# Performance work log

Hardware: AMD Instinct MI355X
Metric: run time of the kernel (lower is better)

Reference implementation:

```python
import jax, jax.numpy as jnp
import numpy as np

B, N, DIM = 2, 2048, 1024
HEADS, DH, NUM_MEM = 8, 64, 4
EPS = 1e-5


def layer_norm(x, gamma):
    mu = x.mean(-1, keepdims=True)
    var = ((x - mu) ** 2).mean(-1, keepdims=True)
    return (x - mu) * jax.lax.rsqrt(var + EPS) * gamma


def setup_inputs() -> dict:
    key = jax.random.key(0)
    ks = jax.random.split(key, 7)
    x = jax.random.normal(ks[0], (B, N, DIM), jnp.float32)
    mask = jax.random.randint(ks[1], (B, N), 0, 2) > 0
    attn_bias = jax.random.normal(ks[2], (HEADS, N, N), jnp.float32) * 0.02
    gamma = jnp.ones((DIM,), jnp.float32)
    Wq = jax.random.normal(ks[3], (DIM, HEADS * DH), jnp.float32) * (DIM ** -0.5)
    Wkv = jax.random.normal(ks[4], (DIM, 2 * DH), jnp.float32) * (DIM ** -0.5)
    mem_kv = jax.random.normal(ks[5], (2, NUM_MEM, DH), jnp.float32)
    Wout = jax.random.normal(ks[6], (HEADS * DH, DIM), jnp.float32) * ((HEADS * DH) ** -0.5)
    return dict(x=x, attn_bias=attn_bias, gamma=gamma, Wq=Wq, Wkv=Wkv,
                mem_kv=mem_kv, Wout=Wout, mask=mask)


def reference(x, attn_bias, gamma, Wq, Wkv, mem_kv, Wout, mask):
    b, n, _ = x.shape
    # norm applied to query path only; kv comes from pre-norm x (self-attention)
    xn = layer_norm(x, gamma)
    q = (xn @ Wq).reshape(b, n, HEADS, DH).transpose(0, 2, 1, 3) * (DH ** -0.5)  # b h n d
    kv = x @ Wkv  # multi-query: single shared kv head
    k, v = kv[..., :DH], kv[..., DH:]
    mk = jnp.broadcast_to(mem_kv[0], (b, NUM_MEM, DH))
    mv = jnp.broadcast_to(mem_kv[1], (b, NUM_MEM, DH))
    k = jnp.concatenate([mk, k], axis=1)  # b (m+n) d
    v = jnp.concatenate([mv, v], axis=1)
    j = n + NUM_MEM
    bias = jnp.pad(attn_bias, ((0, 0), (0, 0), (NUM_MEM, 0)))  # zero bias on mem tokens
    maskp = jnp.pad(mask, ((0, 0), (NUM_MEM, 0)), constant_values=True)
    sim = jnp.einsum('bhid,bjd->bhij', q, k) + bias
    neg = -jnp.finfo(sim.dtype).max
    sim = jnp.where(maskp[:, None, None, :], sim, neg)
    causal = jnp.triu(jnp.ones((n, j), bool), k=NUM_MEM + 1)  # mem tokens always visible
    sim = jnp.where(causal, neg, sim)
    attn = jax.nn.softmax(sim, axis=-1)
    out = jnp.einsum('bhij,bjd->bhid', attn, v)
    out = out.transpose(0, 2, 1, 3).reshape(b, n, HEADS * DH)
    return out @ Wout
```

## Files before the change

kernel.cpp:

```cpp
#include <hip/hip_runtime.h>
#include <hip/hip_bf16.h>
#include <float.h>

#define B_ 2
#define N_ 2048
#define DIM_ 1024
#define HEADS_ 8
#define DH_ 64
#define NUM_MEM_ 4
#define ROWS_ (B_ * N_)
#define QCOLS_ (HEADS_ * DH_)
#define JTOT_ (N_ + NUM_MEM_)
#define JPAD_ 2176
#define CHUNKS_PER_BH_ 77

typedef __attribute__((ext_vector_type(8))) short short8v;
typedef __attribute__((ext_vector_type(4))) float f32x4;

static __device__ __forceinline__ ushort f2b(float f) {
    __hip_bfloat16 hb = __float2bfloat16(f);
    return *(ushort*)&hb;
}
static __device__ __forceinline__ uint pk2(float a, float b) {
    return ((uint)f2b(b) << 16) | (uint)f2b(a);
}
static __device__ __forceinline__ float b2f_lo(uint u) {
    union { uint x; float f; } c; c.x = u << 16; return c.f;
}
static __device__ __forceinline__ float b2f_hi(uint u) {
    union { uint x; float f; } c; c.x = u & 0xffff0000u; return c.f;
}

__global__ __launch_bounds__(256) void ln_cast_kernel(const float* __restrict__ x,
                                                      const float* __restrict__ gamma,
                                                      ushort* __restrict__ xb,
                                                      ushort* __restrict__ xnb) {
    int row = blockIdx.x;
    const float4 v = ((const float4*)(x + (size_t)row * DIM_))[threadIdx.x];
    float s  = v.x + v.y + v.z + v.w;
    float s2 = v.x * v.x + v.y * v.y + v.z * v.z + v.w * v.w;
    #pragma unroll
    for (int off = 32; off > 0; off >>= 1) {
        s  += __shfl_down(s, off);
        s2 += __shfl_down(s2, off);
    }
    __shared__ float ws1[4], ws2[4];
    int lane = threadIdx.x & 63, wid = threadIdx.x >> 6;
    if (lane == 0) { ws1[wid] = s; ws2[wid] = s2; }
    __syncthreads();
    float tot  = ws1[0] + ws1[1] + ws1[2] + ws1[3];
    float tot2 = ws2[0] + ws2[1] + ws2[2] + ws2[3];
    float mu  = tot * (1.0f / DIM_);
    float var = tot2 * (1.0f / DIM_) - mu * mu;
    float rs  = rsqrtf(var + 1e-5f);
    const float4 g = ((const float4*)gamma)[threadIdx.x];
    float vv[4] = {v.x, v.y, v.z, v.w};
    float gg[4] = {g.x, g.y, g.z, g.w};
    ushort xo[4], xno[4];
    #pragma unroll
    for (int j = 0; j < 4; ++j) {
        xo[j]  = f2b(vv[j]);
        xno[j] = f2b((vv[j] - mu) * rs * gg[j]);
    }
    *(int2*)(xb  + (size_t)row * DIM_ + threadIdx.x * 4) = *(int2*)xo;
    *(int2*)(xnb + (size_t)row * DIM_ + threadIdx.x * 4) = *(int2*)xno;
}

static __device__ __forceinline__ void wtrans_body(const float* __restrict__ W,
                                                   ushort* __restrict__ Wt,
                                                   int K, int N, int t) {
    int n = t % N;
    int k0 = (t / N) * 8;
    ushort u[8];
    #pragma unroll
    for (int j = 0; j < 8; ++j) u[j] = f2b(W[(size_t)(k0 + j) * N + n]);
    *(int4*)(Wt + (size_t)n * K + k0) = *(int4*)u;
}

__global__ __launch_bounds__(256) void prep_kernel(const float* __restrict__ Wq,
                                                   const float* __restrict__ Wkv,
                                                   const float* __restrict__ Wout,
                                                   const float* __restrict__ mem_kv,
                                                   const int* __restrict__ mask,
                                                   ushort* __restrict__ Wqt,
                                                   ushort* __restrict__ Wkvt,
                                                   ushort* __restrict__ Woutt,
                                                   ushort* __restrict__ Kb,
                                                   ushort* __restrict__ Vt,
                                                   ushort* __restrict__ amask) {
    int bid = blockIdx.x;
    int tid = threadIdx.x;
    if (bid < 256) {
        wtrans_body(Wq, Wqt, DIM_, QCOLS_, bid * 256 + tid);
    } else if (bid < 320) {
        wtrans_body(Wkv, Wkvt, DIM_, 2 * DH_, (bid - 256) * 256 + tid);
    } else if (bid < 576) {
        wtrans_body(Wout, Woutt, QCOLS_, DIM_, (bid - 320) * 256 + tid);
    } else if (bid < 640) {
        int t = (bid - 576) * 256 + tid;
        int d  = t & 63;
        int ji = (t >> 6) & 127;
        int b  = t >> 13;
        int j  = (ji < NUM_MEM_) ? ji : (2048 + ji);
        float kv_ = 0.f, vv = 0.f;
        if (ji < NUM_MEM_) {
            kv_ = mem_kv[ji * DH_ + d];
            vv  = mem_kv[NUM_MEM_ * DH_ + ji * DH_ + d];
        }
        Kb[((size_t)(b * JPAD_) + j) * DH_ + d] = f2b(kv_);
        Vt[((size_t)(b * DH_) + d) * JPAD_ + j] = f2b(vv);
    } else {
        int t = (bid - 640) * 256 + tid;
        if (t < B_ * JPAD_) {
            int b = t / JPAD_;
            int j = t % JPAD_;
            float v;
            if (j < NUM_MEM_) v = 0.f;
            else if (j < JTOT_) v = mask[b * N_ + (j - NUM_MEM_)] ? 0.f : -1e30f;
            else v = -1e30f;
            amask[(size_t)b * JPAD_ + j] = f2b(v);
        }
    }
}

template<int MODE, int BM>
__global__ __launch_bounds__(256) void gemm_bf16(const ushort* __restrict__ A,
                                                 const ushort* __restrict__ Bt,
                                                 void* __restrict__ C,
                                                 void* __restrict__ C2,
                                                 int M, int N, int K) {
    constexpr int RT = BM / 64;
    __shared__ ushort As[BM][40];
    __shared__ ushort Bs[64][40];
    int tid = threadIdx.x;
    int w = tid >> 6, l = tid & 63, lg = l >> 4, ll = l & 15;
    int r0 = blockIdx.y * BM, c0 = blockIdx.x * 64;

    int arow = tid >> 2;
    int achk = (tid & 3) * 8;
    const ushort* Ap  = A + (size_t)(r0 + arow) * K + achk;
    const ushort* Ap2 = Ap + (size_t)64 * K;
    const ushort* Bp  = Bt + (size_t)(c0 + arow) * K + achk;

    int4 a0 = *(const int4*)Ap;
    int4 a1;
    if constexpr (RT == 2) a1 = *(const int4*)Ap2;
    int4 b0 = *(const int4*)Bp;

    f32x4 acc[RT][4] = {};

    int nk = K / 32;
    for (int ks = 0; ks < nk; ++ks) {
        __syncthreads();
        *(int4*)&As[arow][achk] = a0;
        if constexpr (RT == 2) *(int4*)&As[arow + 64][achk] = a1;
        *(int4*)&Bs[arow][achk] = b0;
        __syncthreads();
        int kn = (ks + 1 < nk) ? (ks + 1) * 32 : 0;
        a0 = *(const int4*)(Ap + kn);
        if constexpr (RT == 2) a1 = *(const int4*)(Ap2 + kn);
        b0 = *(const int4*)(Bp + kn);
        short8v af[RT], bf[4];
        #pragma unroll
        for (int rt = 0; rt < RT; ++rt)
            af[rt] = *(const short8v*)&As[w * 16 * RT + rt * 16 + ll][lg * 8];
        #pragma unroll
        for (int ct = 0; ct < 4; ++ct)
            bf[ct] = *(const short8v*)&Bs[ct * 16 + ll][lg * 8];
        __builtin_amdgcn_s_setprio(1);
        #pragma unroll
        for (int rt = 0; rt < RT; ++rt)
            #pragma unroll
            for (int ct = 0; ct < 4; ++ct)
                acc[rt][ct] = __builtin_amdgcn_mfma_f32_16x16x32_bf16(af[rt], bf[ct], acc[rt][ct], 0, 0, 0);
        __builtin_amdgcn_s_setprio(0);
    }

    #pragma unroll
    for (int rt = 0; rt < RT; ++rt) {
        #pragma unroll
        for (int ct = 0; ct < 4; ++ct) {
            #pragma unroll
            for (int r = 0; r < 4; ++r) {
                int row = r0 + w * 16 * RT + rt * 16 + lg * 4 + r;
                int col = c0 + ct * 16 + ll;
                float val = acc[rt][ct][r];
                if (MODE == 0) {
                    ((ushort*)C)[(size_t)row * QCOLS_ + col] = f2b(val * 0.125f);
                } else if (MODE == 1) {
                    int b = row >> 11;
                    int j = (row & 2047) + NUM_MEM_;
                    if (col < DH_)
                        ((ushort*)C)[((size_t)(b * JPAD_) + j) * DH_ + col] = f2b(val);
                    else
                        ((ushort*)C2)[((size_t)(b * DH_) + (col - DH_)) * JPAD_ + j] = f2b(val);
                } else {
                    ((float*)C)[(size_t)row * DIM_ + col] = val;
                }
            }
        }
    }
}

__global__ __launch_bounds__(256, 4) void fattn_split_kernel(const ushort* __restrict__ qb,
                                                             const ushort* __restrict__ Kb,
                                                             const ushort* __restrict__ Vt,
                                                             const float* __restrict__ bias,
                                                             const ushort* __restrict__ amask,
                                                             ushort* __restrict__ part_O,
                                                             float* __restrict__ part_ml) {
    __shared__ ushort Ks[64][72];
    __shared__ ushort Vs[64][72];
    __shared__ ushort Pt[4][16][72];
    __shared__ ushort Bb[64][68];

    int cid = blockIdx.x;
    int bh  = cid / CHUNKS_PER_BH_;
    int rem = cid - bh * CHUNKS_PER_BH_;
    int b = bh >> 3, h = bh & 7;
    int qt = 0, ci = 0;
    {
        int cum = 0;
        #pragma unroll 1
        for (int t = 0; t < 32; ++t) {
            int c = (t + 10) / 9;
            if (rem < cum + c) { qt = t; ci = rem - cum; break; }
            cum += c;
        }
    }
    int nt = qt + 2;
    int nc = (qt + 10) / 9;
    int t0 = ci * nt / nc;
    int t1 = (ci + 1) * nt / nc;
    int q0 = qt * 64;

    int tid = threadIdx.x;
    int w  = tid >> 6;
    int l  = tid & 63;
    int lg = l >> 4;
    int ll = l & 15;
    int i_row = q0 + w * 16 + ll;

    short8v aq0, aq1;
    {
        const ushort* qp = qb + ((size_t)(b * N_ + i_row)) * QCOLS_ + h * DH_;
        aq0 = *(const short8v*)(qp + lg * 8);
        aq1 = *(const short8v*)(qp + 32 + lg * 8);
    }

    int trow = tid >> 5;
    int tpc  = tid & 31;
    const float*  bias_rb = bias + ((size_t)h * N_ + q0 + trow) * N_;
    const ushort* am_row  = amask + (size_t)b * JPAD_;

    int sr = tid >> 3, sc = (tid & 7) * 8;
    const ushort* KbB = Kb + (size_t)b * JPAD_ * DH_;
    const ushort* VtB = Vt + (size_t)b * DH_ * JPAD_;

    auto fold_bias = [&](const float2* bv, uint am2, uint* bbx) {
        float amf0 = b2f_lo(am2), amf1 = b2f_hi(am2);
        int j_e = 0;
        (void)j_e;
    };
    (void)fold_bias;

    int jp0 = t0 * 64;
    int4 kr0 = *(const int4*)(KbB + (size_t)(jp0 + sr) * DH_ + sc);
    int4 kr1 = *(const int4*)(KbB + (size_t)(jp0 + sr + 32) * DH_ + sc);
    int4 vr0 = *(const int4*)(VtB + (size_t)sr * JPAD_ + jp0 + sc);
    int4 vr1 = *(const int4*)(VtB + (size_t)(sr + 32) * JPAD_ + jp0 + sc);

    uint bbc[8];
    {
        int j_e = jp0 + 2 * tpc;
        int sj  = j_e - NUM_MEM_;
        int sjc = sj < 0 ? 0 : (sj > N_ - 2 ? N_ - 2 : sj);
        uint am2 = *(const uint*)(am_row + j_e);
        float amf0 = b2f_lo(am2), amf1 = b2f_hi(am2);
        #pragma unroll
        for (int p = 0; p < 8; ++p) {
            float2 bv = *(const float2*)(bias_rb + (size_t)(8 * p) * N_ + sjc);
            int i_s = q0 + trow + 8 * p;
            float v0 = (j_e     < NUM_MEM_) ? 0.f : bv.x + amf0;
            float v1 = (j_e + 1 < NUM_MEM_) ? 0.f : bv.y + amf1;
            v0 = (j_e     <= i_s + NUM_MEM_) ? v0 : -1e30f;
            v1 = (j_e + 1 <= i_s + NUM_MEM_) ? v1 : -1e30f;
            bbc[p] = pk2(v0, v1);
        }
    }

    f32x4 oacc[4] = {};
    float mrow1 = -1e30f, lsum1 = 0.f;

    for (int jt = t0; jt < t1; ++jt) {
        __syncthreads();
        *(int4*)&Ks[sr][sc]      = kr0;
        *(int4*)&Ks[sr + 32][sc] = kr1;
        *(int4*)&Vs[sr][sc]      = vr0;
        *(int4*)&Vs[sr + 32][sc] = vr1;
        #pragma unroll
        for (int p = 0; p < 8; ++p)
            *(uint*)&Bb[trow + 8 * p][2 * tpc] = bbc[p];
        __syncthreads();

        int jn0 = (jt + 1 < t1 ? jt + 1 : jt) * 64;
        kr0 = *(const int4*)(KbB + (size_t)(jn0 + sr) * DH_ + sc);
        kr1 = *(const int4*)(KbB + (size_t)(jn0 + sr + 32) * DH_ + sc);
        vr0 = *(const int4*)(VtB + (size_t)sr * JPAD_ + jn0 + sc);
        vr1 = *(const int4*)(VtB + (size_t)(sr + 32) * JPAD_ + jn0 + sc);
        int j_e = jn0 + 2 * tpc;
        int sj  = j_e - NUM_MEM_;
        int sjc = sj < 0 ? 0 : (sj > N_ - 2 ? N_ - 2 : sj);
        uint am2n = *(const uint*)(am_row + j_e);
        float2 bvn[8];
        #pragma unroll
        for (int p = 0; p < 8; ++p)
            bvn[p] = *(const float2*)(bias_rb + (size_t)(8 * p) * N_ + sjc);

        float s[4][4];
        #pragma unroll
        for (int ct = 0; ct < 4; ++ct) {
            f32x4 acc = {};
            short8v bk0 = *(const short8v*)&Ks[ct * 16 + ll][lg * 8];
            short8v bk1 = *(const short8v*)&Ks[ct * 16 + ll][32 + lg * 8];
            __builtin_amdgcn_s_setprio(1);
            acc = __builtin_amdgcn_mfma_f32_16x16x32_bf16(bk0, aq0, acc, 0, 0, 0);
            acc = __builtin_amdgcn_mfma_f32_16x16x32_bf16(bk1, aq1, acc, 0, 0, 0);
            __builtin_amdgcn_s_setprio(0);
            uint2 ub = *(const uint2*)&Bb[w * 16 + ll][ct * 16 + lg * 4];
            s[ct][0] = acc[0] + b2f_lo(ub.x);
            s[ct][1] = acc[1] + b2f_hi(ub.x);
            s[ct][2] = acc[2] + b2f_lo(ub.y);
            s[ct][3] = acc[3] + b2f_hi(ub.y);
        }

        float m01 = fmaxf(fmaxf(s[0][0], s[0][1]), fmaxf(s[0][2], s[0][3]));
        float m23 = fmaxf(fmaxf(s[1][0], s[1][1]), fmaxf(s[1][2], s[1][3]));
        float m45 = fmaxf(fmaxf(s[2][0], s[2][1]), fmaxf(s[2][2], s[2][3]));
        float m67 = fmaxf(fmaxf(s[3][0], s[3][1]), fmaxf(s[3][2], s[3][3]));
        float m = fmaxf(fmaxf(m01, m23), fmaxf(m45, m67));
        m = fmaxf(m, __shfl_xor(m, 16));
        m = fmaxf(m, __shfl_xor(m, 32));
        float mn = fmaxf(mrow1, m);
        float scl = __expf(mrow1 - mn);
        mrow1 = mn;

        float ps = 0.f;
        #pragma unroll
        for (int ct = 0; ct < 4; ++ct)
            #pragma unroll
            for (int r = 0; r < 4; ++r) {
                float p = __expf(s[ct][r] - mn);
                s[ct][r] = p;
                ps += p;
            }
        ps += __shfl_xor(ps, 16);
        ps += __shfl_xor(ps, 32);
        lsum1 = lsum1 * scl + ps;

        #pragma unroll
        for (int ct = 0; ct < 4; ++ct) {
            uint2 pu;
            pu.x = pk2(s[ct][0], s[ct][1]);
            pu.y = pk2(s[ct][2], s[ct][3]);
            *(uint2*)&Pt[w][ll][ct * 16 + lg * 4] = pu;
        }
        #pragma unroll
        for (int dt = 0; dt < 4; ++dt)
            #pragma unroll
            for (int r = 0; r < 4; ++r) oacc[dt][r] *= scl;

        #pragma unroll
        for (int c = 0; c < 2; ++c) {
            short8v ptf = *(const short8v*)&Pt[w][ll][c * 32 + lg * 8];
            __builtin_amdgcn_s_setprio(1);
            #pragma unroll
            for (int dt = 0; dt < 4; ++dt) {
                short8v bv = *(const short8v*)&Vs[dt * 16 + ll][c * 32 + lg * 8];
                oacc[dt] = __builtin_amdgcn_mfma_f32_16x16x32_bf16(bv, ptf, oacc[dt], 0, 0, 0);
            }
            __builtin_amdgcn_s_setprio(0);
        }

        {
            float amf0 = b2f_lo(am2n), amf1 = b2f_hi(am2n);
            #pragma unroll
            for (int p = 0; p < 8; ++p) {
                int i_s = q0 + trow + 8 * p;
                float v0 = (j_e     < NUM_MEM_) ? 0.f : bvn[p].x + amf0;
                float v1 = (j_e + 1 < NUM_MEM_) ? 0.f : bvn[p].y + amf1;
                v0 = (j_e     <= i_s + NUM_MEM_) ? v0 : -1e30f;
                v1 = (j_e + 1 <= i_s + NUM_MEM_) ? v1 : -1e30f;
                bbc[p] = pk2(v0, v1);
            }
        }
    }

    int slot = (bh * 32 + qt) * 4 + ci;
    ushort* po = part_O + (size_t)slot * 4096;
    #pragma unroll
    for (int dt = 0; dt < 4; ++dt) {
        uint2 pu;
        pu.x = pk2(oacc[dt][0], oacc[dt][1]);
        pu.y = pk2(oacc[dt][2], oacc[dt][3]);
        *(uint2*)&po[(w * 16 + ll) * 64 + dt * 16 + lg * 4] = pu;
    }
    if (lg == 0) {
        part_ml[(size_t)slot * 128 + (w * 16 + ll) * 2]     = mrow1;
        part_ml[(size_t)slot * 128 + (w * 16 + ll) * 2 + 1] = lsum1;
    }
}

__global__ __launch_bounds__(256) void merge_kernel(const ushort* __restrict__ part_O,
                                                    const float* __restrict__ part_ml,
                                                    ushort* __restrict__ attn_ob) {
    int bid = blockIdx.x;
    int qt = bid & 31;
    int bh = bid >> 5;
    int b = bh >> 3, h = bh & 7;
    int nc = (qt + 10) / 9;
    int tid = threadIdx.x;
    int row = tid >> 2;
    int dseg = (tid & 3) * 16;
    int slot0 = bid * 4;

    float M = -1e30f;
    #pragma unroll
    for (int c = 0; c < 4; ++c) {
        if (c >= nc) break;
        M = fmaxf(M, part_ml[(size_t)(slot0 + c) * 128 + row * 2]);
    }
    float den = 0.f;
    float num[16] = {};
    #pragma unroll
    for (int c = 0; c < 4; ++c) {
        if (c >= nc) break;
        float m_c = part_ml[(size_t)(slot0 + c) * 128 + row * 2];
        float l_c = part_ml[(size_t)(slot0 + c) * 128 + row * 2 + 1];
        float wgt = __expf(m_c - M);
        den += wgt * l_c;
        const uint4* src = (const uint4*)(part_O + (size_t)(slot0 + c) * 4096 + row * 64 + dseg);
        uint4 v0 = src[0];
        uint uu[8] = { v0.x, v0.y, v0.z, v0.w, 0, 0, 0, 0 };
        uint4 v1 = src[1];
        uu[4] = v1.x; uu[5] = v1.y; uu[6] = v1.z; uu[7] = v1.w;
        #pragma unroll
        for (int e = 0; e < 8; ++e) {
            num[e * 2 + 0] += wgt * b2f_lo(uu[e]);
            num[e * 2 + 1] += wgt * b2f_hi(uu[e]);
        }
    }
    float inv = 1.f / den;
    ushort o[16];
    #pragma unroll
    for (int e = 0; e < 16; ++e) o[e] = f2b(num[e] * inv);
    int i = qt * 64 + row;
    ushort* dst = attn_ob + ((size_t)(b * N_ + i)) * QCOLS_ + h * DH_ + dseg;
    *(int4*)dst = *(int4*)o;
    *(int4*)(dst + 8) = *(int4*)(o + 8);
}

extern "C" void kernel_launch(void* const* d_in, const int* in_sizes, int n_in,
                              void* d_out, int out_size, void* d_ws, size_t ws_size,
                              hipStream_t stream) {
    const float* x         = (const float*)d_in[0];
    const float* attn_bias = (const float*)d_in[1];
    const float* gamma     = (const float*)d_in[2];
    const float* Wq        = (const float*)d_in[3];
    const float* Wkv       = (const float*)d_in[4];
    const float* mem_kv    = (const float*)d_in[5];
    const float* Wout      = (const float*)d_in[6];
    const int*   mask      = (const int*)d_in[7];
    float* out = (float*)d_out;

    char* wsb = (char*)d_ws;
    ushort* xb      = (ushort*)wsb;
    ushort* xnb     = (ushort*)(wsb + (8u  << 20));
    ushort* qb      = (ushort*)(wsb + (16u << 20));
    ushort* attn_ob = (ushort*)(wsb + (20u << 20));
    ushort* Kb      = (ushort*)(wsb + (24u << 20));
    ushort* Vt      = (ushort*)(wsb + (25u << 20));
    ushort* Wqt     = (ushort*)(wsb + (26u << 20));
    ushort* Wkvt    = (ushort*)(wsb + (27u << 20));
    ushort* Woutt   = (ushort*)(wsb + (28u << 20));
    ushort* amask   = (ushort*)(wsb + (29u << 20));
    ushort* part_O  = (ushort*)(wsb + (32u << 20));
    float*  part_ml = (float*)(wsb + (64u << 20));

    ln_cast_kernel<<<ROWS_, 256, 0, stream>>>(x, gamma, xb, xnb);
    prep_kernel<<<657, 256, 0, stream>>>(Wq, Wkv, Wout, mem_kv, mask, Wqt, Wkvt, Woutt, Kb, Vt, amask);

    gemm_bf16<0, 64><<<dim3(QCOLS_ / 64, ROWS_ / 64), 256, 0, stream>>>(xnb, Wqt, qb, nullptr, ROWS_, QCOLS_, DIM_);
    gemm_bf16<1, 64><<<dim3((2 * DH_) / 64, ROWS_ / 64), 256, 0, stream>>>(xb, Wkvt, Kb, Vt, ROWS_, 2 * DH_, DIM_);
    fattn_split_kernel<<<16 * CHUNKS_PER_BH_, 256, 0, stream>>>(qb, Kb, Vt, attn_bias, amask, part_O, part_ml);
    merge_kernel<<<512, 256, 0, stream>>>(part_O, part_ml, attn_ob);
    gemm_bf16<2, 128><<<dim3(DIM_ / 64, ROWS_ / 128), 256, 0, stream>>>(attn_ob, Woutt, out, nullptr, ROWS_, DIM_, QCOLS_);
}
```

Before: 103.2 us.

## Merge launch stages and replace LDS P transpose with lane shuffles

```diff
diff --git a/kernel.cpp b/kernel.cpp
--- a/kernel.cpp
+++ b/kernel.cpp
@@ -31,41 +31,6 @@
     union { uint x; float f; } c; c.x = u & 0xffff0000u; return c.f;
 }
 
-__global__ __launch_bounds__(256) void ln_cast_kernel(const float* __restrict__ x,
-                                                      const float* __restrict__ gamma,
-                                                      ushort* __restrict__ xb,
-                                                      ushort* __restrict__ xnb) {
-    int row = blockIdx.x;
-    const float4 v = ((const float4*)(x + (size_t)row * DIM_))[threadIdx.x];
-    float s  = v.x + v.y + v.z + v.w;
-    float s2 = v.x * v.x + v.y * v.y + v.z * v.z + v.w * v.w;
-    #pragma unroll
-    for (int off = 32; off > 0; off >>= 1) {
-        s  += __shfl_down(s, off);
-        s2 += __shfl_down(s2, off);
-    }
-    __shared__ float ws1[4], ws2[4];
-    int lane = threadIdx.x & 63, wid = threadIdx.x >> 6;
-    if (lane == 0) { ws1[wid] = s; ws2[wid] = s2; }
-    __syncthreads();
-    float tot  = ws1[0] + ws1[1] + ws1[2] + ws1[3];
-    float tot2 = ws2[0] + ws2[1] + ws2[2] + ws2[3];
-    float mu  = tot * (1.0f / DIM_);
-    float var = tot2 * (1.0f / DIM_) - mu * mu;
-    float rs  = rsqrtf(var + 1e-5f);
-    const float4 g = ((const float4*)gamma)[threadIdx.x];
-    float vv[4] = {v.x, v.y, v.z, v.w};
-    float gg[4] = {g.x, g.y, g.z, g.w};
-    ushort xo[4], xno[4];
-    #pragma unroll
-    for (int j = 0; j < 4; ++j) {
-        xo[j]  = f2b(vv[j]);
-        xno[j] = f2b((vv[j] - mu) * rs * gg[j]);
-    }
-    *(int2*)(xb  + (size_t)row * DIM_ + threadIdx.x * 4) = *(int2*)xo;
-    *(int2*)(xnb + (size_t)row * DIM_ + threadIdx.x * 4) = *(int2*)xno;
-}
-
 static __device__ __forceinline__ void wtrans_body(const float* __restrict__ W,
                                                    ushort* __restrict__ Wt,
                                                    int K, int N, int t) {
@@ -77,18 +42,55 @@
     *(int4*)(Wt + (size_t)n * K + k0) = *(int4*)u;
 }
 
-__global__ __launch_bounds__(256) void prep_kernel(const float* __restrict__ Wq,
-                                                   const float* __restrict__ Wkv,
-                                                   const float* __restrict__ Wout,
-                                                   const float* __restrict__ mem_kv,
-                                                   const int* __restrict__ mask,
-                                                   ushort* __restrict__ Wqt,
-                                                   ushort* __restrict__ Wkvt,
-                                                   ushort* __restrict__ Woutt,
-                                                   ushort* __restrict__ Kb,
-                                                   ushort* __restrict__ Vt,
-                                                   ushort* __restrict__ amask) {
-    int bid = blockIdx.x;
+__global__ __launch_bounds__(256) void ln_prep_kernel(const float* __restrict__ x,
+                                                      const float* __restrict__ gamma,
+                                                      const float* __restrict__ Wq,
+                                                      const float* __restrict__ Wkv,
+                                                      const float* __restrict__ Wout,
+                                                      const float* __restrict__ mem_kv,
+                                                      const int* __restrict__ mask,
+                                                      ushort* __restrict__ xb,
+                                                      ushort* __restrict__ xnb,
+                                                      ushort* __restrict__ Wqt,
+                                                      ushort* __restrict__ Wkvt,
+                                                      ushort* __restrict__ Woutt,
+                                                      ushort* __restrict__ Kb,
+                                                      ushort* __restrict__ Vt,
+                                                      ushort* __restrict__ amask) {
+    int bid0 = blockIdx.x;
+    if (bid0 < ROWS_) {
+        int row = bid0;
+        const float4 v = ((const float4*)(x + (size_t)row * DIM_))[threadIdx.x];
+        float s  = v.x + v.y + v.z + v.w;
+        float s2 = v.x * v.x + v.y * v.y + v.z * v.z + v.w * v.w;
+        #pragma unroll
+        for (int off = 32; off > 0; off >>= 1) {
+            s  += __shfl_down(s, off);
+            s2 += __shfl_down(s2, off);
+        }
+        __shared__ float ws1[4], ws2[4];
+        int lane = threadIdx.x & 63, wid = threadIdx.x >> 6;
+        if (lane == 0) { ws1[wid] = s; ws2[wid] = s2; }
+        __syncthreads();
+        float tot  = ws1[0] + ws1[1] + ws1[2] + ws1[3];
+        float tot2 = ws2[0] + ws2[1] + ws2[2] + ws2[3];
+        float mu  = tot * (1.0f / DIM_);
+        float var = tot2 * (1.0f / DIM_) - mu * mu;
+        float rs  = rsqrtf(var + 1e-5f);
+        const float4 g = ((const float4*)gamma)[threadIdx.x];
+        float vv[4] = {v.x, v.y, v.z, v.w};
+        float gg[4] = {g.x, g.y, g.z, g.w};
+        ushort xo[4], xno[4];
+        #pragma unroll
+        for (int j = 0; j < 4; ++j) {
+            xo[j]  = f2b(vv[j]);
+            xno[j] = f2b((vv[j] - mu) * rs * gg[j]);
+        }
+        *(int2*)(xb  + (size_t)row * DIM_ + threadIdx.x * 4) = *(int2*)xo;
+        *(int2*)(xnb + (size_t)row * DIM_ + threadIdx.x * 4) = *(int2*)xno;
+        return;
+    }
+    int bid = bid0 - ROWS_;
     int tid = threadIdx.x;
     if (bid < 256) {
         wtrans_body(Wq, Wqt, DIM_, QCOLS_, bid * 256 + tid);
@@ -123,18 +125,96 @@
     }
 }
 
-template<int MODE, int BM>
-__global__ __launch_bounds__(256) void gemm_bf16(const ushort* __restrict__ A,
-                                                 const ushort* __restrict__ Bt,
-                                                 void* __restrict__ C,
-                                                 void* __restrict__ C2,
-                                                 int M, int N, int K) {
-    constexpr int RT = BM / 64;
-    __shared__ ushort As[BM][40];
+template<int MODE>
+static __device__ __forceinline__ void gemm64_body(ushort (*As)[40], ushort (*Bs)[40],
+                                                   const ushort* __restrict__ A,
+                                                   const ushort* __restrict__ Bt,
+                                                   void* __restrict__ C,
+                                                   void* __restrict__ C2,
+                                                   int N, int K, int bx, int by) {
+    int tid = threadIdx.x;
+    int w = tid >> 6, l = tid & 63, lg = l >> 4, ll = l & 15;
+    int r0 = by * 64, c0 = bx * 64;
+
+    int arow = tid >> 2;
+    int achk = (tid & 3) * 8;
+    const ushort* Ap = A + (size_t)(r0 + arow) * K + achk;
+    const ushort* Bp = Bt + (size_t)(c0 + arow) * K + achk;
+
+    int4 a0 = *(const int4*)Ap;
+    int4 b0 = *(const int4*)Bp;
+
+    f32x4 acc[4] = {};
+
+    int nk = K / 32;
+    for (int ks = 0; ks < nk; ++ks) {
+        __syncthreads();
+        *(int4*)&As[arow][achk] = a0;
+        *(int4*)&Bs[arow][achk] = b0;
+        __syncthreads();
+        int kn = (ks + 1 < nk) ? (ks + 1) * 32 : 0;
+        a0 = *(const int4*)(Ap + kn);
+        b0 = *(const int4*)(Bp + kn);
+        short8v af, bf[4];
+        af = *(const short8v*)&As[w * 16 + ll][lg * 8];
+        #pragma unroll
+        for (int ct = 0; ct < 4; ++ct)
+            bf[ct] = *(const short8v*)&Bs[ct * 16 + ll][lg * 8];
+        __builtin_amdgcn_s_setprio(1);
+        #pragma unroll
+        for (int ct = 0; ct < 4; ++ct)
+            acc[ct] = __builtin_amdgcn_mfma_f32_16x16x32_bf16(af, bf[ct], acc[ct], 0, 0, 0);
+        __builtin_amdgcn_s_setprio(0);
+    }
+
+    #pragma unroll
+    for (int ct = 0; ct < 4; ++ct) {
+        #pragma unroll
+        for (int r = 0; r < 4; ++r) {
+            int row = r0 + w * 16 + lg * 4 + r;
+            int col = c0 + ct * 16 + ll;
+            float val = acc[ct][r];
+            if (MODE == 0) {
+                ((ushort*)C)[(size_t)row * QCOLS_ + col] = f2b(val * 0.125f);
+            } else {
+                int b = row >> 11;
+                int j = (row & 2047) + NUM_MEM_;
+                if (col < DH_)
+                    ((ushort*)C)[((size_t)(b * JPAD_) + j) * DH_ + col] = f2b(val);
+                else
+                    ((ushort*)C2)[((size_t)(b * DH_) + (col - DH_)) * JPAD_ + j] = f2b(val);
+            }
+        }
+    }
+}
+
+__global__ __launch_bounds__(256) void gemm01_kernel(const ushort* __restrict__ xnb,
+                                                     const ushort* __restrict__ Wqt,
+                                                     ushort* __restrict__ qb,
+                                                     const ushort* __restrict__ xb,
+                                                     const ushort* __restrict__ Wkvt,
+                                                     ushort* __restrict__ Kb,
+                                                     ushort* __restrict__ Vt) {
+    __shared__ ushort As[64][40];
+    __shared__ ushort Bs[64][40];
+    int bid = blockIdx.x;
+    if (bid < 512) {
+        gemm64_body<0>(As, Bs, xnb, Wqt, qb, nullptr, QCOLS_, DIM_, bid & 7, bid >> 3);
+    } else {
+        int r = bid - 512;
+        gemm64_body<1>(As, Bs, xb, Wkvt, Kb, Vt, 2 * DH_, DIM_, r & 1, r >> 1);
+    }
+}
+
+__global__ __launch_bounds__(256) void gemm_out_kernel(const ushort* __restrict__ A,
+                                                       const ushort* __restrict__ Bt,
+                                                       float* __restrict__ C,
+                                                       int M, int N, int K) {
+    __shared__ ushort As[128][40];
     __shared__ ushort Bs[64][40];
     int tid = threadIdx.x;
     int w = tid >> 6, l = tid & 63, lg = l >> 4, ll = l & 15;
-    int r0 = blockIdx.y * BM, c0 = blockIdx.x * 64;
+    int r0 = blockIdx.y * 128, c0 = blockIdx.x * 64;
 
     int arow = tid >> 2;
     int achk = (tid & 3) * 8;
@@ -143,33 +223,31 @@
     const ushort* Bp  = Bt + (size_t)(c0 + arow) * K + achk;
 
     int4 a0 = *(const int4*)Ap;
-    int4 a1;
-    if constexpr (RT == 2) a1 = *(const int4*)Ap2;
+    int4 a1 = *(const int4*)Ap2;
     int4 b0 = *(const int4*)Bp;
 
-    f32x4 acc[RT][4] = {};
+    f32x4 acc[2][4] = {};
 
     int nk = K / 32;
     for (int ks = 0; ks < nk; ++ks) {
         __syncthreads();
-        *(int4*)&As[arow][achk] = a0;
-        if constexpr (RT == 2) *(int4*)&As[arow + 64][achk] = a1;
-        *(int4*)&Bs[arow][achk] = b0;
+        *(int4*)&As[arow][achk]      = a0;
+        *(int4*)&As[arow + 64][achk] = a1;
+        *(int4*)&Bs[arow][achk]      = b0;
         __syncthreads();
         int kn = (ks + 1 < nk) ? (ks + 1) * 32 : 0;
         a0 = *(const int4*)(Ap + kn);
-        if constexpr (RT == 2) a1 = *(const int4*)(Ap2 + kn);
+        a1 = *(const int4*)(Ap2 + kn);
         b0 = *(const int4*)(Bp + kn);
-        short8v af[RT], bf[4];
-        #pragma unroll
-        for (int rt = 0; rt < RT; ++rt)
-            af[rt] = *(const short8v*)&As[w * 16 * RT + rt * 16 + ll][lg * 8];
+        short8v af[2], bf[4];
+        af[0] = *(const short8v*)&As[w * 32 + ll][lg * 8];
+        af[1] = *(const short8v*)&As[w * 32 + 16 + ll][lg * 8];
         #pragma unroll
         for (int ct = 0; ct < 4; ++ct)
             bf[ct] = *(const short8v*)&Bs[ct * 16 + ll][lg * 8];
         __builtin_amdgcn_s_setprio(1);
         #pragma unroll
-        for (int rt = 0; rt < RT; ++rt)
+        for (int rt = 0; rt < 2; ++rt)
             #pragma unroll
             for (int ct = 0; ct < 4; ++ct)
                 acc[rt][ct] = __builtin_amdgcn_mfma_f32_16x16x32_bf16(af[rt], bf[ct], acc[rt][ct], 0, 0, 0);
@@ -177,29 +255,15 @@
     }
 
     #pragma unroll
-    for (int rt = 0; rt < RT; ++rt) {
-        #pragma unroll
-        for (int ct = 0; ct < 4; ++ct) {
+    for (int rt = 0; rt < 2; ++rt)
+        #pragma unroll
+        for (int ct = 0; ct < 4; ++ct)
             #pragma unroll
             for (int r = 0; r < 4; ++r) {
-                int row = r0 + w * 16 * RT + rt * 16 + lg * 4 + r;
+                int row = r0 + w * 32 + rt * 16 + lg * 4 + r;
                 int col = c0 + ct * 16 + ll;
-                float val = acc[rt][ct][r];
-                if (MODE == 0) {
-                    ((ushort*)C)[(size_t)row * QCOLS_ + col] = f2b(val * 0.125f);
-                } else if (MODE == 1) {
-                    int b = row >> 11;
-                    int j = (row & 2047) + NUM_MEM_;
-                    if (col < DH_)
-                        ((ushort*)C)[((size_t)(b * JPAD_) + j) * DH_ + col] = f2b(val);
-                    else
-                        ((ushort*)C2)[((size_t)(b * DH_) + (col - DH_)) * JPAD_ + j] = f2b(val);
-                } else {
-                    ((float*)C)[(size_t)row * DIM_ + col] = val;
-                }
+                C[(size_t)row * DIM_ + col] = acc[rt][ct][r];
             }
-        }
-    }
 }
 
 __global__ __launch_bounds__(256, 4) void fattn_split_kernel(const ushort* __restrict__ qb,
@@ -211,7 +275,6 @@
                                                              float* __restrict__ part_ml) {
     __shared__ ushort Ks[64][72];
     __shared__ ushort Vs[64][72];
-    __shared__ ushort Pt[4][16][72];
     __shared__ ushort Bb[64][68];
 
     int cid = blockIdx.x;
@@ -257,12 +320,9 @@
     const ushort* KbB = Kb + (size_t)b * JPAD_ * DH_;
     const ushort* VtB = Vt + (size_t)b * DH_ * JPAD_;
 
-    auto fold_bias = [&](const float2* bv, uint am2, uint* bbx) {
-        float amf0 = b2f_lo(am2), amf1 = b2f_hi(am2);
-        int j_e = 0;
-        (void)j_e;
-    };
-    (void)fold_bias;
+    int srcA = ((l & 16) << 1) + ll;
+    int srcB = srcA + 16;
+    bool hi = (l & 32) != 0;
 
     int jp0 = t0 * 64;
     int4 kr0 = *(const int4*)(KbB + (size_t)(jp0 + sr) * DH_ + sc);
@@ -358,12 +418,11 @@
         ps += __shfl_xor(ps, 32);
         lsum1 = lsum1 * scl + ps;
 
+        uint pux[4], puy[4];
         #pragma unroll
         for (int ct = 0; ct < 4; ++ct) {
-            uint2 pu;
-            pu.x = pk2(s[ct][0], s[ct][1]);
-            pu.y = pk2(s[ct][2], s[ct][3]);
-            *(uint2*)&Pt[w][ll][ct * 16 + lg * 4] = pu;
+            pux[ct] = pk2(s[ct][0], s[ct][1]);
+            puy[ct] = pk2(s[ct][2], s[ct][3]);
         }
         #pragma unroll
         for (int dt = 0; dt < 4; ++dt)
@@ -372,7 +431,21 @@
 
         #pragma unroll
         for (int c = 0; c < 2; ++c) {
-            short8v ptf = *(const short8v*)&Pt[w][ll][c * 32 + lg * 8];
+            int cl = 2 * c, ch = 2 * c + 1;
+            uint xA_l = (uint)__shfl((int)pux[cl], srcA);
+            uint xA_h = (uint)__shfl((int)pux[ch], srcA);
+            uint yA_l = (uint)__shfl((int)puy[cl], srcA);
+            uint yA_h = (uint)__shfl((int)puy[ch], srcA);
+            uint xB_l = (uint)__shfl((int)pux[cl], srcB);
+            uint xB_h = (uint)__shfl((int)pux[ch], srcB);
+            uint yB_l = (uint)__shfl((int)puy[cl], srcB);
+            uint yB_h = (uint)__shfl((int)puy[ch], srcB);
+            uint uu[4];
+            uu[0] = hi ? xA_h : xA_l;
+            uu[1] = hi ? yA_h : yA_l;
+            uu[2] = hi ? xB_h : xB_l;
+            uu[3] = hi ? yB_h : yB_l;
+            short8v ptf = *(const short8v*)uu;
             __builtin_amdgcn_s_setprio(1);
             #pragma unroll
             for (int dt = 0; dt < 4; ++dt) {
@@ -441,9 +514,8 @@
         den += wgt * l_c;
         const uint4* src = (const uint4*)(part_O + (size_t)(slot0 + c) * 4096 + row * 64 + dseg);
         uint4 v0 = src[0];
-        uint uu[8] = { v0.x, v0.y, v0.z, v0.w, 0, 0, 0, 0 };
         uint4 v1 = src[1];
-        uu[4] = v1.x; uu[5] = v1.y; uu[6] = v1.z; uu[7] = v1.w;
+        uint uu[8] = { v0.x, v0.y, v0.z, v0.w, v1.x, v1.y, v1.z, v1.w };
         #pragma unroll
         for (int e = 0; e < 8; ++e) {
             num[e * 2 + 0] += wgt * b2f_lo(uu[e]);
@@ -487,12 +559,10 @@
     ushort* part_O  = (ushort*)(wsb + (32u << 20));
     float*  part_ml = (float*)(wsb + (64u << 20));
 
-    ln_cast_kernel<<<ROWS_, 256, 0, stream>>>(x, gamma, xb, xnb);
-    prep_kernel<<<657, 256, 0, stream>>>(Wq, Wkv, Wout, mem_kv, mask, Wqt, Wkvt, Woutt, Kb, Vt, amask);
-
-    gemm_bf16<0, 64><<<dim3(QCOLS_ / 64, ROWS_ / 64), 256, 0, stream>>>(xnb, Wqt, qb, nullptr, ROWS_, QCOLS_, DIM_);
-    gemm_bf16<1, 64><<<dim3((2 * DH_) / 64, ROWS_ / 64), 256, 0, stream>>>(xb, Wkvt, Kb, Vt, ROWS_, 2 * DH_, DIM_);
+    ln_prep_kernel<<<ROWS_ + 657, 256, 0, stream>>>(x, gamma, Wq, Wkv, Wout, mem_kv, mask,
+                                                    xb, xnb, Wqt, Wkvt, Woutt, Kb, Vt, amask);
+    gemm01_kernel<<<640, 256, 0, stream>>>(xnb, Wqt, qb, xb, Wkvt, Kb, Vt);
     fattn_split_kernel<<<16 * CHUNKS_PER_BH_, 256, 0, stream>>>(qb, Kb, Vt, attn_bias, amask, part_O, part_ml);
     merge_kernel<<<512, 256, 0, stream>>>(part_O, part_ml, attn_ob);
-    gemm_bf16<2, 128><<<dim3(DIM_ / 64, ROWS_ / 128), 256, 0, stream>>>(attn_ob, Woutt, out, nullptr, ROWS_, DIM_, QCOLS_);
-}
+    gemm_out_kernel<<<dim3(DIM_ / 64, ROWS_ / 128), 256, 0, stream>>>(attn_ob, Woutt, out, ROWS_, DIM_, QCOLS_);
+}
```

After: 94.89 us. 8.1% less time.
